# Optimization experiments

Hardware: AMD Instinct MI355X
Metric: run time of the kernel (lower is better)

Reference implementation:

```python
import jax, jax.numpy as jnp
import numpy as np

# ---- geometry / physics constants (from init_kwargs) ----
nx, NX = 96, 192
dx, nt, dt = 1.0, 200, 0.3
nm, sr, sR = 32, 4, 70
fc, sgma, t0, bg = 0.5, 1.0, 3.0, 1.5
abc_pd = NX // 2 - sR - 1          # 25
pd = (NX - nx) // 2 - abc_pd       # 23
TOT = pd + abc_pd                  # total pad on each side

_thetas = 2 * np.pi * np.arange(nm) / nm
_mx = (NX / 2 + sR * np.cos(_thetas)).astype(int)
_my = (NX / 2 + sR * np.sin(_thetas)).astype(int)
MEAS = jnp.asarray(NX * _mx + _my)            # (nm,) flat receiver indices
TRANS = jnp.asarray((NX * _mx + _my)[::sr])   # (nr,) flat source indices
NR = int(TRANS.shape[0])                      # 8 source channels

_times = np.arange(nt) * dt
SRC = jnp.asarray(np.sin(2 * np.pi * fc * _times) * np.exp(-(_times - t0) ** 2 / (2 * sgma ** 2)), dtype=jnp.float32)

# background field: bg everywhere except outer abc ring of width abc_pd = 1e-6
_bgf = np.full((NX, NX), 1e-6, dtype=np.float32)
_bgf[abc_pd:-abc_pd, abc_pd:-abc_pd] = bg
BGF = jnp.asarray(_bgf)[None, None]           # (1,1,NX,NX)


def lap4(p):
    """4th-order 5-point stencil Laplacian with periodic (roll) wrap, matching torch.roll."""
    r = lambda s, a: jnp.roll(p, s, axis=a)
    lx = (-r(2, -2) + 16 * r(1, -2) - 30 * p + 16 * r(-1, -2) - r(-2, -2)) / 12
    ly = (-r(2, -1) + 16 * r(1, -1) - 30 * p + 16 * r(-1, -1) - r(-2, -1)) / 12
    return lx + ly


def compute_P0():
    """HelperFoward on the homogeneous bg medium: background wavefield (1,NR,nt,NX,NX)."""
    coef = (dt * BGF / dx) ** 2
    amp = (bg * dt / dx) ** 2
    ch = jnp.arange(NR)

    def step(carry, s):
        p0, p1 = carry
        p = 2 * p1 - p0 + coef * lap4(p1)
        pf = p.reshape(1, NR, NX * NX)
        pf = pf.at[:, ch, TRANS].add(amp * s)   # one source pixel per channel (eye)
        p = pf.reshape(1, NR, NX, NX)
        return (p1, p), p

    z = jnp.zeros((1, NR, NX, NX), jnp.float32)
    _, ps = jax.lax.scan(step, (z, z), SRC)      # (nt,1,NR,NX,NX)
    return jnp.transpose(ps, (1, 2, 0, 3, 4))    # (1,NR,nt,NX,NX)


def setup_inputs() -> dict:
    key = jax.random.key(0)
    # sound-speed map around bg=1.5 (must be positive; module computes bg/x)
    x = bg + 0.1 * (jax.random.uniform(key, (2, 1, nx, nx), jnp.float32) - 0.5)
    P0 = compute_P0()
    return {"x": x, "P0": P0}


def reference(x, P0):
    B = x.shape[0]
    xx = bg / x
    # both pads use value 1 -> single constant pad of width TOT
    X = jnp.pad(xx, ((0, 0), (0, 0), (TOT, TOT), (TOT, TOT)), constant_values=1.0)
    coef = (dt * BGF / dx) ** 2                          # (1,1,NX,NX)
    rf = (BGF / bg) ** 2 * (1.0 - X ** 2)                # (B,1,NX,NX)
    # second time-difference of the background field; zero for j<2
    P0t = jnp.transpose(P0, (2, 0, 1, 3, 4))             # (nt,1,NR,NX,NX)
    d2 = jnp.zeros_like(P0t).at[2:].set(P0t[2:] - 2 * P0t[1:-1] + P0t[:-2])

    def step(carry, d2j):
        p0, p1 = carry
        p = 2 * p1 - p0 + coef * lap4(p1) + rf * d2j     # (B,NR,NX,NX)
        meas = p.reshape(B, NR, NX * NX)[:, :, MEAS]     # (B,NR,nm)
        return (p1, p), meas

    z = jnp.zeros((B, NR, NX, NX), x.dtype)
    _, outs = jax.lax.scan(step, (z, z), d2)             # (nt,B,NR,nm)
    return jnp.transpose(outs, (1, 2, 3, 0))             # (B,NR,nm,nt)
```

## Files before the change

### kernel.cpp

```cpp
#include <hip/hip_runtime.h>
#include <math.h>

#define NXg      192
#define PLANE_SZ (NXg*NXg)
#define PLANES   16
#define TOTAL    (PLANES*PLANE_SZ)
#define NT       200
#define NM       32
#define CW       96
#define C0       48
#define W96SQ    (CW*CW)
#define A0       24
#define TILE     36
#define HALO     20
#define EXPW     76
#define LSTR     84
#define KSTEP    10
#define NLAUNCH  20
#define NSB      (38*19)
#define BLK      768

struct MeasIdx { int v[NM]; };
typedef float4 f4;
typedef float2 f2;

__device__ __forceinline__ void barrier_lds(){
    asm volatile("s_waitcnt lgkmcnt(0)\n\ts_barrier" ::: "memory");
}

__device__ __forceinline__ f4 frow2(f2 L, f4 C, f2 Q,
                                    f4 m2, f4 m1, f4 p1, f4 p2,
                                    f4 O, f4 CFs, f4 RF, f4 D2)
{
    f4 r;
    {
        float s16 = (L.y + C.y) + (m1.x + p1.x);
        float s1  = (L.x + C.z) + (m2.x + p2.x);
        float st  = fmaf(16.f, s16, -s1);
        st = fmaf(-60.f, C.x, st);
        float p = fmaf(2.f, C.x, -O.x);
        p = fmaf(CFs.x, st, p);
        r.x = fmaf(RF.x, D2.x, p);
    }
    {
        float s16 = (C.x + C.z) + (m1.y + p1.y);
        float s1  = (L.y + C.w) + (m2.y + p2.y);
        float st  = fmaf(16.f, s16, -s1);
        st = fmaf(-60.f, C.y, st);
        float p = fmaf(2.f, C.y, -O.y);
        p = fmaf(CFs.y, st, p);
        r.y = fmaf(RF.y, D2.y, p);
    }
    {
        float s16 = (C.y + C.w) + (m1.z + p1.z);
        float s1  = (C.x + Q.x) + (m2.z + p2.z);
        float st  = fmaf(16.f, s16, -s1);
        st = fmaf(-60.f, C.z, st);
        float p = fmaf(2.f, C.z, -O.z);
        p = fmaf(CFs.z, st, p);
        r.z = fmaf(RF.z, D2.z, p);
    }
    {
        float s16 = (C.z + Q.x) + (m1.w + p1.w);
        float s1  = (C.y + Q.y) + (m2.w + p2.w);
        float st  = fmaf(16.f, s16, -s1);
        st = fmaf(-60.f, C.w, st);
        float p = fmaf(2.f, C.w, -O.w);
        p = fmaf(CFs.w, st, p);
        r.w = fmaf(RF.w, D2.w, p);
    }
    return r;
}

__device__ __forceinline__ f4 d2c(f4 c, f4 b, f4 a){
    f4 r;
    r.x = c.x - 2.f*b.x + a.x;
    r.y = c.y - 2.f*b.y + a.y;
    r.z = c.z - 2.f*b.z + a.z;
    r.w = c.w - 2.f*b.w + a.w;
    return r;
}

__global__ __launch_bounds__(BLK, 3)
void step_fused(const float* __restrict__ RA, const float* __restrict__ RB,
                float* __restrict__ WA, float* __restrict__ WB,
                const float* __restrict__ P0, const float* __restrict__ x,
                float* __restrict__ out, int J, MeasIdx meas)
{
    __shared__ float lds0[EXPW*LSTR];
    __shared__ float lds1[EXPW*LSTR];
    const int tid = threadIdx.x;
    const int sw  = ((blockIdx.x & 7) << 5) | (blockIdx.x >> 3);
    const int pl  = sw >> 4;
    const int t   = sw & 15;
    const int ty  = t >> 2, tx = t & 3;
    const int gy0 = A0 + ty*TILE - HALO;
    const int gx0 = A0 + tx*TILE - HALO;
    const int b   = pl >> 3, rch = pl & 7;
    const size_t pbase = (size_t)pl * PLANE_SZ;
    const f4 z4 = make_float4(0.f,0.f,0.f,0.f);

    {
        const bool zf = (J == 0);
        for (int i = tid; i < EXPW*19; i += BLK){
            int ly = i/19, lx4 = (i%19)*4;
            int gyr = gy0 + ly, gxg = gx0 + lx4;
            bool ok = !zf && ((unsigned)(gyr - A0) < 144u)
                          && ((unsigned)(gxg - A0) < 144u);
            f4 vb = z4;
            if (ok){
                vb = *(const f4*)&RB[pbase + (size_t)gyr*NXg + gxg];
            }
            lds1[ly*LSTR + lx4    ] = vb.x;
            *(f4*)&lds1[ly*LSTR + lx4] = vb;
        }
        if (zf){
            for (int i = tid; i < EXPW*LSTR; i += BLK)
                if ((i % LSTR) >= EXPW) lds1[i] = 0.f;
        }
    }

    const bool val = (tid < NSB);
    const int gg  = val ? tid : 0;
    const int sby = gg/19, sbx = gg%19;
    const int ly0 = 2*sby, lx0 = 4*sbx;
    const int oC  = ly0*LSTR + lx0;
    int s1 = (ly0-1) >> 1;
    int s2 = (73-ly0) >> 1;
    int s3 = (lx0+1) >> 1;
    int s4 = (73-lx0) >> 1;
    const int sMax = val ? min(min(s1,s2), min(s3,s4)) : -1;
    const int gy = gy0 + ly0, gx = gx0 + lx0;
    const bool win = (gy>=C0 && gy<C0+CW && gx>=C0 && gx<C0+CW);
    const int pofs = win ? (gy*NXg + gx) : 0;
    const bool act = ((unsigned)(gy - A0) < 144u) && ((unsigned)(gx - A0) < 144u);

    f4 OA0 = z4, OA1 = z4;
    if (val && act && J > 0){
        const float* rp = RA + pbase + (size_t)gy*NXg + gx;
        OA0 = *(const f4*)rp;
        OA1 = *(const f4*)(rp + NXg);
    }

    f4 rfa, rfb2;
    if (win){
        const float* xp = x + (size_t)b*W96SQ + (size_t)(gy-C0)*CW + (gx-C0);
        f4 x0 = *(const f4*)xp;
        f4 x1 = *(const f4*)(xp + CW);
        float tq;
        tq = 1.5f/x0.x; rfa.x  = 1.0f - tq*tq;
        tq = 1.5f/x0.y; rfa.y  = 1.0f - tq*tq;
        tq = 1.5f/x0.z; rfa.z  = 1.0f - tq*tq;
        tq = 1.5f/x0.w; rfa.w  = 1.0f - tq*tq;
        tq = 1.5f/x1.x; rfb2.x = 1.0f - tq*tq;
        tq = 1.5f/x1.y; rfb2.y = 1.0f - tq*tq;
        tq = 1.5f/x1.z; rfb2.z = 1.0f - tq*tq;
        tq = 1.5f/x1.w; rfb2.w = 1.0f - tq*tq;
    } else {
        rfa = z4; rfb2 = z4;
    }
    f4 cfa, cfb;
    {
        float c0v[4], c1v[4];
#pragma unroll
        for (int ii=0; ii<4; ++ii){
            int gxr = gx + ii;
            bool ix = (gxr>=25 && gxr<167);
            float g0 = 0.3f * ((ix && gy  >=25 && gy  <167) ? 1.5f : 1e-6f);
            float g1 = 0.3f * ((ix && gy+1>=25 && gy+1<167) ? 1.5f : 1e-6f);
            c0v[ii] = (g0*g0)*(1.0f/12.0f);
            c1v[ii] = (g1*g1)*(1.0f/12.0f);
        }
        cfa = make_float4(c0v[0],c0v[1],c0v[2],c0v[3]);
        cfb = make_float4(c1v[0],c1v[1],c1v[2],c1v[3]);
    }

    bool own = false; int loff = 0; size_t obase = 0;
    if (tid < NM){
        int rv = meas.v[tid];
        int ry = rv / NXg, rx = rv % NXg;
        int dy = ry - (A0 + ty*TILE), dx = rx - (A0 + tx*TILE);
        own = ((unsigned)dy < TILE) && ((unsigned)dx < TILE);
        loff = (dy+HALO)*LSTR + (dx+HALO);
        obase = ((size_t)pl*NM + tid)*NT;
    }

    const float* P0r = P0 + (size_t)rch*NT*PLANE_SZ;
    f4 Pa0=z4, Pa1=z4, Pb0=z4, Pb1=z4, D0=z4, D1=z4;
    if (win){
        const float* p = P0r + (size_t)J*PLANE_SZ + pofs;
        Pa0 = *(const f4*)p;
        Pa1 = *(const f4*)(p + NXg);
        if (J >= 1){
            Pb0 = *(const f4*)(p - PLANE_SZ);
            Pb1 = *(const f4*)(p - PLANE_SZ + NXg);
        }
        if (J >= 2){
            f4 Pc0 = *(const f4*)(p - 2*PLANE_SZ);
            f4 Pc1 = *(const f4*)(p - 2*PLANE_SZ + NXg);
            D0 = d2c(Pa0, Pb0, Pc0);
            D1 = d2c(Pa1, Pb1, Pc1);
        }
    }

    barrier_lds();

    f4 OB0 = *(const f4*)&lds1[oC];
    f4 OB1 = *(const f4*)&lds1[oC+LSTR];

#pragma unroll
    for (int s=0; s<KSTEP; ++s){
        float* pa = (s&1) ? lds1 : lds0;
        float* pb = (s&1) ? lds0 : lds1;

        const bool pre = (s+1 < KSTEP) && win && ((s+1) <= sMax);
        f4 Pn0 = z4, Pn1 = z4;
        if (pre){
            const float* p = P0r + (size_t)(J+s+1)*PLANE_SZ + pofs;
            Pn0 = *(const f4*)p;
            Pn1 = *(const f4*)(p + NXg);
        }

        if (s <= sMax){
            f4 C0r = (s&1) ? OA0 : OB0;
            f4 C1r = (s&1) ? OA1 : OB1;
            f4 O0  = (s&1) ? OB0 : OA0;
            f4 O1  = (s&1) ? OB1 : OA1;
            f4 Rm2 = *(const f4*)&pb[oC - 2*LSTR];
            f4 Rm1 = *(const f4*)&pb[oC -   LSTR];
            f4 Rp2 = *(const f4*)&pb[oC + 2*LSTR];
            f4 Rp3 = *(const f4*)&pb[oC + 3*LSTR];
            f2 L0  = *(const f2*)&pb[oC - 2];
            f2 L1  = *(const f2*)&pb[oC + LSTR - 2];
            f2 Q0  = *(const f2*)&pb[oC + 4];
            f2 Q1  = *(const f2*)&pb[oC + LSTR + 4];
            f4 N0 = frow2(L0, C0r, Q0, Rm2, Rm1, C1r, Rp2, O0, cfa, rfa,  D0);
            f4 N1 = frow2(L1, C1r, Q1, Rm1, C0r, Rp2, Rp3, O1, cfb, rfb2, D1);
            *(f4*)&pa[oC]        = N0;
            *(f4*)&pa[oC + LSTR] = N1;
            if (s&1){ OB0=N0; OB1=N1; } else { OA0=N0; OA1=N1; }
        }

        barrier_lds();

        if (pre){
            if (J+s+1 >= 2){
                D0 = d2c(Pn0, Pa0, Pb0);
                D1 = d2c(Pn1, Pa1, Pb1);
            } else { D0 = z4; D1 = z4; }
            Pb0 = Pa0; Pb1 = Pa1;
            Pa0 = Pn0; Pa1 = Pn1;
        }

        if (own) out[obase + (J+s)] = pa[loff];
    }

    if (J != (NLAUNCH-1)*KSTEP){
        for (int i = tid; i < TILE*(TILE/4); i += BLK){
            int r = i/9, c4 = (i%9)*4;
            size_t go = pbase + (size_t)(A0 + ty*TILE + r)*NXg + (A0 + tx*TILE + c4);
            int lo = (r+HALO)*LSTR + (c4+HALO);
            *(f4*)&WB[go] = *(const f4*)&lds1[lo];
            *(f4*)&WA[go] = *(const f4*)&lds0[lo];
        }
    }
}

extern "C" void kernel_launch(void* const* d_in, const int* in_sizes, int n_in,
                              void* d_out, int out_size, void* d_ws, size_t ws_size,
                              hipStream_t stream)
{
    const float* x  = (const float*)d_in[0];
    const float* P0 = (const float*)d_in[1];
    float* out = (float*)d_out;

    float* F   = (float*)d_ws;
    float* f0  = F;
    float* f1  = F + (size_t)TOTAL;
    float* f2p = F + 2*(size_t)TOTAL;
    float* f3p = F + 3*(size_t)TOTAL;

    MeasIdx meas;
    for (int k=0;k<NM;++k){
        double th = 2.0*M_PI*(double)k/(double)NM;
        int mx = (int)(96.0 + 70.0*cos(th));
        int my = (int)(96.0 + 70.0*sin(th));
        meas.v[k] = mx*NXg + my;
    }

    float *RA=f0, *RB=f1, *WA=f2p, *WB=f3p;
    for (int L=0; L<NLAUNCH; ++L){
        step_fused<<<256, BLK, 0, stream>>>(RA,RB,WA,WB,P0,x,out,L*KSTEP,meas);
        float* tsw;
        tsw=RA; RA=WA; WA=tsw;
        tsw=RB; RB=WB; WB=tsw;
    }
}
```

Before: 228.9 us.

## Compute 4x4 register sub-blocks per thread instead of 2x4 in fused stencil

Each thread now updates a 4-row by 4-column patch rather than 2 rows, halving the thread count to 512 per block and reusing more vertically adjacent values from registers instead of LDS reads. The block size and launch bounds are reduced accordingly (2 blocks per CU), and the explicit LDS zeroing of pad columns on the first launch is dropped. This cuts LDS traffic per output point but raises register pressure and lowers occupancy; the sMax edge bound was also changed, which may alter which halo cells are valid.

```diff
diff --git a/kernel.cpp b/kernel.cpp
--- a/kernel.cpp
+++ b/kernel.cpp
@@ -8,7 +8,7 @@
 #define NT       200
 #define NM       32
 #define CW       96
-#define C0       48
+#define WIN0     48
 #define W96SQ    (CW*CW)
 #define A0       24
 #define TILE     36
@@ -17,8 +17,8 @@
 #define LSTR     84
 #define KSTEP    10
 #define NLAUNCH  20
-#define NSB      (38*19)
-#define BLK      768
+#define NSB      (19*19)
+#define BLK      512
 
 struct MeasIdx { int v[NM]; };
 typedef float4 f4;
@@ -81,7 +81,7 @@
     return r;
 }
 
-__global__ __launch_bounds__(BLK, 3)
+__global__ __launch_bounds__(BLK, 2)
 void step_fused(const float* __restrict__ RA, const float* __restrict__ RB,
                 float* __restrict__ WA, float* __restrict__ WB,
                 const float* __restrict__ P0, const float* __restrict__ x,
@@ -108,71 +108,70 @@
             bool ok = !zf && ((unsigned)(gyr - A0) < 144u)
                           && ((unsigned)(gxg - A0) < 144u);
             f4 vb = z4;
-            if (ok){
-                vb = *(const f4*)&RB[pbase + (size_t)gyr*NXg + gxg];
-            }
-            lds1[ly*LSTR + lx4    ] = vb.x;
+            if (ok) vb = *(const f4*)&RB[pbase + (size_t)gyr*NXg + gxg];
             *(f4*)&lds1[ly*LSTR + lx4] = vb;
-        }
-        if (zf){
-            for (int i = tid; i < EXPW*LSTR; i += BLK)
-                if ((i % LSTR) >= EXPW) lds1[i] = 0.f;
         }
     }
 
     const bool val = (tid < NSB);
     const int gg  = val ? tid : 0;
-    const int sby = gg/19, sbx = gg%19;
-    const int ly0 = 2*sby, lx0 = 4*sbx;
+    const int sbr = gg/19, sbx = gg%19;
+    const int ly0 = 4*sbr, lx0 = 4*sbx;
     const int oC  = ly0*LSTR + lx0;
-    int s1 = (ly0-1) >> 1;
-    int s2 = (73-ly0) >> 1;
-    int s3 = (lx0+1) >> 1;
-    int s4 = (73-lx0) >> 1;
-    const int sMax = val ? min(min(s1,s2), min(s3,s4)) : -1;
+    int e1 = (ly0+1) >> 1;
+    int e2 = (73-ly0) >> 1;
+    int e3 = (lx0+1) >> 1;
+    int e4 = (73-lx0) >> 1;
+    const int sMax = val ? min(min(e1,e2), min(e3,e4)) : -1;
     const int gy = gy0 + ly0, gx = gx0 + lx0;
-    const bool win = (gy>=C0 && gy<C0+CW && gx>=C0 && gx<C0+CW);
+    const bool win = ((unsigned)(gy - WIN0) < (unsigned)CW)
+                  && ((unsigned)(gx - WIN0) < (unsigned)CW);
     const int pofs = win ? (gy*NXg + gx) : 0;
     const bool act = ((unsigned)(gy - A0) < 144u) && ((unsigned)(gx - A0) < 144u);
 
-    f4 OA0 = z4, OA1 = z4;
+    f4 OA0=z4, OA1=z4, OA2=z4, OA3=z4;
     if (val && act && J > 0){
         const float* rp = RA + pbase + (size_t)gy*NXg + gx;
         OA0 = *(const f4*)rp;
         OA1 = *(const f4*)(rp + NXg);
-    }
-
-    f4 rfa, rfb2;
+        OA2 = *(const f4*)(rp + 2*NXg);
+        OA3 = *(const f4*)(rp + 3*NXg);
+    }
+
+    f4 rf0=z4, rf1=z4, rf2=z4, rf3=z4;
     if (win){
-        const float* xp = x + (size_t)b*W96SQ + (size_t)(gy-C0)*CW + (gx-C0);
-        f4 x0 = *(const f4*)xp;
-        f4 x1 = *(const f4*)(xp + CW);
-        float tq;
-        tq = 1.5f/x0.x; rfa.x  = 1.0f - tq*tq;
-        tq = 1.5f/x0.y; rfa.y  = 1.0f - tq*tq;
-        tq = 1.5f/x0.z; rfa.z  = 1.0f - tq*tq;
-        tq = 1.5f/x0.w; rfa.w  = 1.0f - tq*tq;
-        tq = 1.5f/x1.x; rfb2.x = 1.0f - tq*tq;
-        tq = 1.5f/x1.y; rfb2.y = 1.0f - tq*tq;
-        tq = 1.5f/x1.z; rfb2.z = 1.0f - tq*tq;
-        tq = 1.5f/x1.w; rfb2.w = 1.0f - tq*tq;
-    } else {
-        rfa = z4; rfb2 = z4;
-    }
-    f4 cfa, cfb;
-    {
-        float c0v[4], c1v[4];
+        const float* xp = x + (size_t)b*W96SQ + (size_t)(gy-WIN0)*CW + (gx-WIN0);
+        f4 xv; float tq;
+        xv = *(const f4*)xp;
+        tq=1.5f/xv.x; rf0.x=1.f-tq*tq; tq=1.5f/xv.y; rf0.y=1.f-tq*tq;
+        tq=1.5f/xv.z; rf0.z=1.f-tq*tq; tq=1.5f/xv.w; rf0.w=1.f-tq*tq;
+        xv = *(const f4*)(xp + CW);
+        tq=1.5f/xv.x; rf1.x=1.f-tq*tq; tq=1.5f/xv.y; rf1.y=1.f-tq*tq;
+        tq=1.5f/xv.z; rf1.z=1.f-tq*tq; tq=1.5f/xv.w; rf1.w=1.f-tq*tq;
+        xv = *(const f4*)(xp + 2*CW);
+        tq=1.5f/xv.x; rf2.x=1.f-tq*tq; tq=1.5f/xv.y; rf2.y=1.f-tq*tq;
+        tq=1.5f/xv.z; rf2.z=1.f-tq*tq; tq=1.5f/xv.w; rf2.w=1.f-tq*tq;
+        xv = *(const f4*)(xp + 3*CW);
+        tq=1.5f/xv.x; rf3.x=1.f-tq*tq; tq=1.5f/xv.y; rf3.y=1.f-tq*tq;
+        tq=1.5f/xv.z; rf3.z=1.f-tq*tq; tq=1.5f/xv.w; rf3.w=1.f-tq*tq;
+    }
+    f4 cf0, cf1, cf2, cf3;
+    {
+        float v[4][4];
 #pragma unroll
-        for (int ii=0; ii<4; ++ii){
-            int gxr = gx + ii;
-            bool ix = (gxr>=25 && gxr<167);
-            float g0 = 0.3f * ((ix && gy  >=25 && gy  <167) ? 1.5f : 1e-6f);
-            float g1 = 0.3f * ((ix && gy+1>=25 && gy+1<167) ? 1.5f : 1e-6f);
-            c0v[ii] = (g0*g0)*(1.0f/12.0f);
-            c1v[ii] = (g1*g1)*(1.0f/12.0f);
-        }
-        cfa = make_float4(c0v[0],c0v[1],c0v[2],c0v[3]);
-        cfb = make_float4(c1v[0],c1v[1],c1v[2],c1v[3]);
+        for (int rr=0; rr<4; ++rr){
+#pragma unroll
+            for (int ii=0; ii<4; ++ii){
+                int gxr = gx + ii, gyr = gy + rr;
+                bool in = (gxr>=25 && gxr<167 && gyr>=25 && gyr<167);
+                float g = 0.3f * (in ? 1.5f : 1e-6f);
+                v[rr][ii] = (g*g)*(1.0f/12.0f);
+            }
+        }
+        cf0 = make_float4(v[0][0],v[0][1],v[0][2],v[0][3]);
+        cf1 = make_float4(v[1][0],v[1][1],v[1][2],v[1][3]);
+        cf2 = make_float4(v[2][0],v[2][1],v[2][2],v[2][3]);
+        cf3 = make_float4(v[3][0],v[3][1],v[3][2],v[3][3]);
     }
 
     bool own = false; int loff = 0; size_t obase = 0;
@@ -186,20 +185,29 @@
     }
 
     const float* P0r = P0 + (size_t)rch*NT*PLANE_SZ;
-    f4 Pa0=z4, Pa1=z4, Pb0=z4, Pb1=z4, D0=z4, D1=z4;
+    f4 Pa0=z4,Pa1=z4,Pa2=z4,Pa3=z4, Pb0=z4,Pb1=z4,Pb2=z4,Pb3=z4;
+    f4 Dr0=z4,Dr1=z4,Dr2=z4,Dr3=z4;
     if (win){
         const float* p = P0r + (size_t)J*PLANE_SZ + pofs;
         Pa0 = *(const f4*)p;
         Pa1 = *(const f4*)(p + NXg);
+        Pa2 = *(const f4*)(p + 2*NXg);
+        Pa3 = *(const f4*)(p + 3*NXg);
         if (J >= 1){
             Pb0 = *(const f4*)(p - PLANE_SZ);
             Pb1 = *(const f4*)(p - PLANE_SZ + NXg);
+            Pb2 = *(const f4*)(p - PLANE_SZ + 2*NXg);
+            Pb3 = *(const f4*)(p - PLANE_SZ + 3*NXg);
         }
         if (J >= 2){
             f4 Pc0 = *(const f4*)(p - 2*PLANE_SZ);
             f4 Pc1 = *(const f4*)(p - 2*PLANE_SZ + NXg);
-            D0 = d2c(Pa0, Pb0, Pc0);
-            D1 = d2c(Pa1, Pb1, Pc1);
+            f4 Pc2 = *(const f4*)(p - 2*PLANE_SZ + 2*NXg);
+            f4 Pc3 = *(const f4*)(p - 2*PLANE_SZ + 3*NXg);
+            Dr0 = d2c(Pa0, Pb0, Pc0);
+            Dr1 = d2c(Pa1, Pb1, Pc1);
+            Dr2 = d2c(Pa2, Pb2, Pc2);
+            Dr3 = d2c(Pa3, Pb3, Pc3);
         }
     }
 
@@ -207,6 +215,8 @@
 
     f4 OB0 = *(const f4*)&lds1[oC];
     f4 OB1 = *(const f4*)&lds1[oC+LSTR];
+    f4 OB2 = *(const f4*)&lds1[oC+2*LSTR];
+    f4 OB3 = *(const f4*)&lds1[oC+3*LSTR];
 
 #pragma unroll
     for (int s=0; s<KSTEP; ++s){
@@ -214,42 +224,59 @@
         float* pb = (s&1) ? lds0 : lds1;
 
         const bool pre = (s+1 < KSTEP) && win && ((s+1) <= sMax);
-        f4 Pn0 = z4, Pn1 = z4;
+        f4 Pn0=z4, Pn1=z4, Pn2=z4, Pn3=z4;
         if (pre){
             const float* p = P0r + (size_t)(J+s+1)*PLANE_SZ + pofs;
             Pn0 = *(const f4*)p;
             Pn1 = *(const f4*)(p + NXg);
+            Pn2 = *(const f4*)(p + 2*NXg);
+            Pn3 = *(const f4*)(p + 3*NXg);
         }
 
         if (s <= sMax){
-            f4 C0r = (s&1) ? OA0 : OB0;
-            f4 C1r = (s&1) ? OA1 : OB1;
-            f4 O0  = (s&1) ? OB0 : OA0;
-            f4 O1  = (s&1) ? OB1 : OA1;
+            f4 Cr0 = (s&1) ? OA0 : OB0;
+            f4 Cr1 = (s&1) ? OA1 : OB1;
+            f4 Cr2 = (s&1) ? OA2 : OB2;
+            f4 Cr3 = (s&1) ? OA3 : OB3;
+            f4 Oo0 = (s&1) ? OB0 : OA0;
+            f4 Oo1 = (s&1) ? OB1 : OA1;
+            f4 Oo2 = (s&1) ? OB2 : OA2;
+            f4 Oo3 = (s&1) ? OB3 : OA3;
             f4 Rm2 = *(const f4*)&pb[oC - 2*LSTR];
             f4 Rm1 = *(const f4*)&pb[oC -   LSTR];
-            f4 Rp2 = *(const f4*)&pb[oC + 2*LSTR];
-            f4 Rp3 = *(const f4*)&pb[oC + 3*LSTR];
+            f4 Rp4 = *(const f4*)&pb[oC + 4*LSTR];
+            f4 Rp5 = *(const f4*)&pb[oC + 5*LSTR];
             f2 L0  = *(const f2*)&pb[oC - 2];
-            f2 L1  = *(const f2*)&pb[oC + LSTR - 2];
+            f2 L1  = *(const f2*)&pb[oC +   LSTR - 2];
+            f2 L2  = *(const f2*)&pb[oC + 2*LSTR - 2];
+            f2 L3  = *(const f2*)&pb[oC + 3*LSTR - 2];
             f2 Q0  = *(const f2*)&pb[oC + 4];
-            f2 Q1  = *(const f2*)&pb[oC + LSTR + 4];
-            f4 N0 = frow2(L0, C0r, Q0, Rm2, Rm1, C1r, Rp2, O0, cfa, rfa,  D0);
-            f4 N1 = frow2(L1, C1r, Q1, Rm1, C0r, Rp2, Rp3, O1, cfb, rfb2, D1);
-            *(f4*)&pa[oC]        = N0;
-            *(f4*)&pa[oC + LSTR] = N1;
-            if (s&1){ OB0=N0; OB1=N1; } else { OA0=N0; OA1=N1; }
+            f2 Q1  = *(const f2*)&pb[oC +   LSTR + 4];
+            f2 Q2  = *(const f2*)&pb[oC + 2*LSTR + 4];
+            f2 Q3  = *(const f2*)&pb[oC + 3*LSTR + 4];
+            f4 N0 = frow2(L0, Cr0, Q0, Rm2, Rm1, Cr1, Cr2, Oo0, cf0, rf0, Dr0);
+            f4 N1 = frow2(L1, Cr1, Q1, Rm1, Cr0, Cr2, Cr3, Oo1, cf1, rf1, Dr1);
+            f4 N2 = frow2(L2, Cr2, Q2, Cr0, Cr1, Cr3, Rp4, Oo2, cf2, rf2, Dr2);
+            f4 N3 = frow2(L3, Cr3, Q3, Cr1, Cr2, Rp4, Rp5, Oo3, cf3, rf3, Dr3);
+            *(f4*)&pa[oC]          = N0;
+            *(f4*)&pa[oC +   LSTR] = N1;
+            *(f4*)&pa[oC + 2*LSTR] = N2;
+            *(f4*)&pa[oC + 3*LSTR] = N3;
+            if (s&1){ OB0=N0; OB1=N1; OB2=N2; OB3=N3; }
+            else    { OA0=N0; OA1=N1; OA2=N2; OA3=N3; }
         }
 
         barrier_lds();
 
         if (pre){
             if (J+s+1 >= 2){
-                D0 = d2c(Pn0, Pa0, Pb0);
-                D1 = d2c(Pn1, Pa1, Pb1);
-            } else { D0 = z4; D1 = z4; }
-            Pb0 = Pa0; Pb1 = Pa1;
-            Pa0 = Pn0; Pa1 = Pn1;
+                Dr0 = d2c(Pn0, Pa0, Pb0);
+                Dr1 = d2c(Pn1, Pa1, Pb1);
+                Dr2 = d2c(Pn2, Pa2, Pb2);
+                Dr3 = d2c(Pn3, Pa3, Pb3);
+            } else { Dr0=z4; Dr1=z4; Dr2=z4; Dr3=z4; }
+            Pb0=Pa0; Pb1=Pa1; Pb2=Pa2; Pb3=Pa3;
+            Pa0=Pn0; Pa1=Pn1; Pa2=Pn2; Pa3=Pn3;
         }
 
         if (own) out[obase + (J+s)] = pa[loff];
```

New measurement: 276.4 us. 20.8% more time.
